# Kernel optimization log

Measured on AMD Instinct MI355X. Metric: run time of the kernel, lower is better.

Reference implementation:

```python
import jax, jax.numpy as jnp
import numpy as np

B, T, C = 4, 2048, 1024
N_HEAD = 16
HEAD_DIM = C // N_HEAD


def setup_inputs() -> dict:
    key = jax.random.key(0)
    k1, k2, k3 = jax.random.split(key, 3)
    x = jax.random.normal(k1, (B, T, C), dtype=jnp.float32)
    w_attn = jax.random.normal(k2, (C, 3 * C), dtype=jnp.float32) * 0.02
    b_attn = jnp.zeros((3 * C,), dtype=jnp.float32)
    # c_proj init stddev = 0.02 / sqrt(2 * n_layer), n_layer = 24
    w_proj = jax.random.normal(k3, (C, C), dtype=jnp.float32) * (0.02 / np.sqrt(48.0))
    b_proj = jnp.zeros((C,), dtype=jnp.float32)
    return {"x": x, "w_attn": w_attn, "b_attn": b_attn,
            "w_proj": w_proj, "b_proj": b_proj}


def reference(x, w_attn, b_attn, w_proj, b_proj):
    Bx, Tx, Cx = x.shape
    scale = 1.0 / jnp.sqrt(jnp.asarray(HEAD_DIM, dtype=x.dtype))
    qkv = x @ w_attn + b_attn                      # [B,T,3C]
    qkv = qkv.reshape(Bx, Tx, 3, N_HEAD, HEAD_DIM)
    q, k, v = qkv[:, :, 0], qkv[:, :, 1], qkv[:, :, 2]  # each [B,T,H,D]
    att = jnp.einsum('bthd,bThd->bhtT', q, k) * scale   # [B,H,T,T]
    mask = jnp.tril(jnp.ones((Tx, Tx), dtype=x.dtype)).reshape(1, 1, Tx, Tx)
    att = att * mask - 1e10 * (1 - mask)
    att = jax.nn.softmax(att, axis=-1)
    y = jnp.einsum('bhtT,bThd->bthd', att, v)      # [B,T,H,D]
    y = y.reshape(Bx, Tx, Cx)
    return y @ w_proj + b_proj
```

## Files before the change

kernel.cpp:

```cpp
#include <hip/hip_runtime.h>
#include <hip/hip_bf16.h>


typedef __attribute__((ext_vector_type(8)))  __bf16 bf16x8;
typedef __attribute__((ext_vector_type(2)))  float  f32x2;
typedef __attribute__((ext_vector_type(4)))  float  f32x4;
typedef __attribute__((ext_vector_type(16))) float  f32x16;
typedef __attribute__((ext_vector_type(4)))  unsigned int u32x4;

#define AS1C(p) ((const __attribute__((address_space(1))) unsigned int*)(p))
#define AS3(p)  ((__attribute__((address_space(3))) unsigned int*)(p))

__device__ __forceinline__ unsigned short f2bfu(float f){
  __hip_bfloat16 h = __float2bfloat16(f);
  return __builtin_bit_cast(unsigned short, h);
}

__device__ __forceinline__ void plswapu(unsigned int &a, unsigned int &b){
  asm("v_permlane32_swap_b32 %0, %1" : "+v"(a), "+v"(b));
}
__device__ __forceinline__ unsigned int cvtpk(float lo, float hi){
  unsigned int r;
  asm("v_cvt_pk_bf16_f32 %0, %1, %2" : "=v"(r) : "v"(lo), "v"(hi));
  return r;
}
__device__ __forceinline__ float max3f(float a, float b, float c){
  float r;
  asm("v_max3_f32 %0, %1, %2, %3" : "=v"(r) : "v"(a), "v"(b), "v"(c));
  return r;
}


__global__ __launch_bounds__(256)
void prep_all(const float* __restrict__ x, __hip_bfloat16* __restrict__ xb,
              const float* __restrict__ w_attn, __hip_bfloat16* __restrict__ wattnT,
              const float* __restrict__ w_proj, __hip_bfloat16* __restrict__ wprojT)
{
  __shared__ float tile[32][33];
  const int idx = blockIdx.x;
  if (idx < 2048){
    const int n4 = 8388608/4;
    for (int i = idx*256 + threadIdx.x; i < n4; i += 2048*256){
      float4 v = reinterpret_cast<const float4*>(x)[i];
      ushort4 u;
      u.x = f2bfu(v.x); u.y = f2bfu(v.y); u.z = f2bfu(v.z); u.w = f2bfu(v.w);
      reinterpret_cast<ushort4*>(xb)[i] = u;
    }
  } else {
    const float* in; __hip_bfloat16* out; int C, R, bx, by;
    if (idx < 5120){
      const int f = idx - 2048;
      in = w_attn; out = wattnT; R = 1024; C = 3072;
      bx = f % 96; by = f / 96;
    } else {
      const int f = idx - 5120;
      in = w_proj; out = wprojT; R = 1024; C = 1024;
      bx = f & 31; by = f >> 5;
    }
    const int tx = threadIdx.x & 31, ty = threadIdx.x >> 5;
    const int c0 = bx*32, r0 = by*32;
    for (int i = ty; i < 32; i += 8)
      tile[i][tx] = in[(size_t)(r0+i)*C + c0 + tx];
    __syncthreads();
    for (int i = ty; i < 32; i += 8)
      out[(size_t)(c0+i)*R + r0 + tx] = __float2bfloat16(tile[tx][i]);
  }
}


#define QSCALE 0.1803368801111244f

__device__ __forceinline__ void stage_ab(const __hip_bfloat16* __restrict__ A,
                                         const __hip_bfloat16* __restrict__ Bt,
                                         int m0, int n0, int K, int kt,
                                         __hip_bfloat16* sA, __hip_bfloat16* sB,
                                         int w, int l)
{
  const int k0 = kt*32;
  #pragma unroll
  for (int qq = 0; qq < 2; ++qq){
    const int c = qq*256 + w*64 + l;
    const int row = c>>2, kc = c&3;
    const int kcs = kc ^ ((row>>1)&3);
    __builtin_amdgcn_global_load_lds(AS1C(A  + (size_t)(m0+row)*K + k0 + 8*kcs),
                                     AS3(sA + (qq*256 + w*64)*8), 16, 0, 0);
    __builtin_amdgcn_global_load_lds(AS1C(Bt + (size_t)(n0+row)*K + k0 + 8*kcs),
                                     AS3(sB + (qq*256 + w*64)*8), 16, 0, 0);
  }
}

template<int EPI>
__global__ __launch_bounds__(256)
void gemm_bf16(const __hip_bfloat16* __restrict__ A,
               const __hip_bfloat16* __restrict__ Bt,
               const float* __restrict__ bias,
               int M, int N, int K,
               __hip_bfloat16* __restrict__ q_s,
               __hip_bfloat16* __restrict__ k_s,
               __hip_bfloat16* __restrict__ vT_s,
               float* __restrict__ outf)
{
  __shared__ __align__(16) __hip_bfloat16 sA[2][128*32];
  __shared__ __align__(16) __hip_bfloat16 sB[2][128*32];
  const int tid = threadIdx.x, w = tid>>6, l = tid&63, g = l>>4, li = l&15;
  const int wm = w>>1, wn = w&1;
  const int sw = (li>>1)&3;

  const int nwg = gridDim.x, cpx = nwg >> 3;
  const int swz = (blockIdx.x & 7)*cpx + (blockIdx.x >> 3);
  const int nbx = N >> 7;
  const int GM = 4, chunk = GM * nbx;
  const int grp = swz / chunk, pos = swz - grp*chunk;
  const int m0 = (grp*GM + (pos & (GM-1)))*128;
  const int n0 = (pos >> 2)*128;

  f32x4 acc[4][4] = {};

  const int NT = K >> 5;
  stage_ab(A, Bt, m0, n0, K, 0, sA[0], sB[0], w, l);
  int cur = 0;

  for (int kt = 0; kt < NT; ++kt){
    __syncthreads();
    if (kt + 1 < NT)
      stage_ab(A, Bt, m0, n0, K, kt+1, sA[cur^1], sB[cur^1], w, l);

    bf16x8 af[4], bfr[4];
    #pragma unroll
    for (int mi = 0; mi < 4; ++mi)
      af[mi] = *reinterpret_cast<const bf16x8*>(sA[cur] + (wm*64 + mi*16 + li)*32 + 8*(g ^ sw));
    #pragma unroll
    for (int ni = 0; ni < 4; ++ni)
      bfr[ni] = *reinterpret_cast<const bf16x8*>(sB[cur] + (wn*64 + ni*16 + li)*32 + 8*(g ^ sw));
    #pragma unroll
    for (int mi = 0; mi < 4; ++mi)
      #pragma unroll
      for (int ni = 0; ni < 4; ++ni)
        acc[mi][ni] = __builtin_amdgcn_mfma_f32_16x16x32_bf16(af[mi], bfr[ni], acc[mi][ni], 0, 0, 0);
    cur ^= 1;
  }

  #pragma unroll
  for (int ni = 0; ni < 4; ++ni){
    const int col = n0 + wn*64 + ni*16 + li;
    const float bv = bias[col];
    #pragma unroll
    for (int mi = 0; mi < 4; ++mi){
      #pragma unroll
      for (int e = 0; e < 4; ++e){
        const int row = m0 + wm*64 + mi*16 + 4*g + e;
        const float val = acc[mi][ni][e] + bv;
        if (EPI == 0){
          const int three = col >> 10, h = (col >> 6) & 15, d = col & 63;
          const int b = row >> 11, t = row & 2047;
          const int bh = b*16 + h;
          if (three == 0)      q_s[((size_t)bh*2048 + t)*64 + d]  = __float2bfloat16(val*QSCALE);
          else if (three == 1) k_s[((size_t)bh*2048 + t)*64 + d]  = __float2bfloat16(val);
          else                 vT_s[((size_t)bh*64 + d)*2048 + t] = __float2bfloat16(val);
        } else {
          outf[(size_t)row*N + col] = val;
        }
      }
    }
  }
}


__device__ __forceinline__ void stage_kv64(const __hip_bfloat16* __restrict__ k_s,
                                           const __hip_bfloat16* __restrict__ vT_s,
                                           size_t base, int j,
                                           __hip_bfloat16* sk, __hip_bfloat16* svt,
                                           int tid)
{
  #pragma unroll
  for (int it = 0; it < 4; ++it){
    const int c = it*128 + tid;
    const int r = c>>3, cc = c&7;
    __builtin_amdgcn_global_load_lds(AS1C(k_s  + base + (size_t)(j*64 + r)*64 + 8*(cc ^ (r&7))),
                                     AS3(sk  + c*8), 16, 0, 0);
    __builtin_amdgcn_global_load_lds(AS1C(vT_s + base + (size_t)r*2048 + j*64 + 8*(cc ^ (r&7))),
                                     AS3(svt + c*8), 16, 0, 0);
  }
}

__device__ __forceinline__ bf16x8 ldtile(const __hip_bfloat16* t, int row, int chunk){
  return *reinterpret_cast<const bf16x8*>(t + row*64 + ((chunk ^ (row&7))*8));
}

__global__ __launch_bounds__(128, 3)
void flash_attn(const __hip_bfloat16* __restrict__ q_s,
                const __hip_bfloat16* __restrict__ k_s,
                const __hip_bfloat16* __restrict__ vT_s,
                __hip_bfloat16* __restrict__ y_s)
{
  __shared__ __align__(16) __hip_bfloat16 sk [2][64*64];
  __shared__ __align__(16) __hip_bfloat16 svt[2][64*64];

  const int tid = threadIdx.x, w = tid>>6, l = tid&63;
  const int lq = l&31, hf = l>>5, h4 = 4*hf;
  const int bid = blockIdx.x;
  const int xcd = bid & 7, sl = (bid>>3) & 7;
  const int v = 31 - (bid >> 6);
  const int bh = xcd*8 + sl;
  const size_t base = (size_t)bh * (2048*64);
  const int b = bh >> 4, hh = bh & 15;

  const int tw = 2*v + w;
  const int jd = v;
  const int qabs = 32*tw + lq;
  const int rel = 32*w + lq;

  bf16x8 qf[4];
  #pragma unroll
  for (int ks = 0; ks < 4; ++ks)
    qf[ks] = *reinterpret_cast<const bf16x8*>(q_s + base + (size_t)qabs*64 + 16*ks + 8*hf);

  f32x16 o0 = {}, o1 = {};
  float mrun = -1e30f, lrun = 0.f;

  stage_kv64(k_s, vT_s, base, 0, sk[0], svt[0], tid);

  #pragma unroll 1
  for (int j = 0; j <= jd; ++j){
    __syncthreads();
    if (j + 1 <= jd)
      stage_kv64(k_s, vT_s, base, j+1, sk[(j+1)&1], svt[(j+1)&1], tid);

    const __hip_bfloat16* skc  = sk[j&1];
    const __hip_bfloat16* svtc = svt[j&1];

    f32x16 s0 = {}, s1 = {};
    __builtin_amdgcn_s_setprio(1);
    #pragma unroll
    for (int ks = 0; ks < 4; ++ks){
      bf16x8 kf0 = ldtile(skc, lq,      2*ks + hf);
      s0 = __builtin_amdgcn_mfma_f32_32x32x16_bf16(kf0, qf[ks], s0, 0, 0, 0);
      bf16x8 kf1 = ldtile(skc, 32 + lq, 2*ks + hf);
      s1 = __builtin_amdgcn_mfma_f32_32x32x16_bf16(kf1, qf[ks], s1, 0, 0, 0);
    }
    __builtin_amdgcn_s_setprio(0);

    f32x2 pf2[16];
    #pragma unroll
    for (int i = 0; i < 8; ++i){
      pf2[i]     = (f32x2){ s0[2*i], s0[2*i+1] };
      pf2[8 + i] = (f32x2){ s1[2*i], s1[2*i+1] };
    }
    if (j == jd){
      #pragma unroll
      for (int i = 0; i < 16; ++i){
        const int a = i >> 3;
        const int r0 = (i & 7)*2, r1 = r0 + 1;
        const int kv0 = 32*a + (r0&3) + 8*(r0>>2) + h4;
        const int kv1 = 32*a + (r1&3) + 8*(r1>>2) + h4;
        pf2[i].x = (kv0 <= rel) ? pf2[i].x : -1e30f;
        pf2[i].y = (kv1 <= rel) ? pf2[i].y : -1e30f;
      }
    }

    #define PFX(K) (((K)&1) ? pf2[(K)>>1].y : pf2[(K)>>1].x)
    float t0 = max3f(PFX(0),PFX(1),PFX(2)),   t1 = max3f(PFX(3),PFX(4),PFX(5));
    float t2 = max3f(PFX(6),PFX(7),PFX(8)),   t3 = max3f(PFX(9),PFX(10),PFX(11));
    float t4 = max3f(PFX(12),PFX(13),PFX(14)),t5 = max3f(PFX(15),PFX(16),PFX(17));
    float t6 = max3f(PFX(18),PFX(19),PFX(20)),t7 = max3f(PFX(21),PFX(22),PFX(23));
    float t8 = max3f(PFX(24),PFX(25),PFX(26)),t9 = max3f(PFX(27),PFX(28),PFX(29));
    float t10 = fmaxf(PFX(30),PFX(31));
    float u0 = max3f(t0,t1,t2), u1 = max3f(t3,t4,t5), u2 = max3f(t6,t7,t8);
    float u3 = fmaxf(t9,t10);
    float pm = fmaxf(max3f(u0,u1,u2), u3);
    #undef PFX

    if (!__all(pm - mrun <= 8.0f)){
      pm = fmaxf(pm, __shfl_xor(pm, 32));
      const float nm = fmaxf(mrun, pm);
      const float corr = exp2f(mrun - nm);
      mrun = nm;
      o0 *= corr; o1 *= corr;
      lrun *= corr;
    }

    const f32x2 negm = { -mrun, -mrun };
    #pragma unroll
    for (int i = 0; i < 16; ++i) pf2[i] = pf2[i] + negm;
    #pragma unroll
    for (int i = 0; i < 16; ++i){
      pf2[i].x = exp2f(pf2[i].x);
      pf2[i].y = exp2f(pf2[i].y);
    }

    f32x2 q8[8];
    #pragma unroll
    for (int i = 0; i < 8; ++i) q8[i] = pf2[i] + pf2[8+i];
    f32x2 q4a = q8[0]+q8[4], q4b = q8[1]+q8[5], q4c = q8[2]+q8[6], q4d = q8[3]+q8[7];
    f32x2 q2a = q4a+q4c, q2b = q4b+q4d;
    f32x2 q1 = q2a+q2b;
    float psum = q1.x + q1.y;
    psum += __shfl_xor(psum, 32);
    lrun += psum;

    unsigned int wds[16];
    #pragma unroll
    for (int k = 0; k < 16; ++k) wds[k] = cvtpk(pf2[k].x, pf2[k].y);
    #pragma unroll
    for (int a = 0; a < 2; ++a)
      #pragma unroll
      for (int bl = 0; bl < 2; ++bl){
        plswapu(wds[a*8 + 4*bl    ], wds[a*8 + 4*bl + 2]);
        plswapu(wds[a*8 + 4*bl + 1], wds[a*8 + 4*bl + 3]);
      }
    bf16x8 pfr[4];
    #pragma unroll
    for (int B = 0; B < 4; ++B){
      u32x4 tt = { wds[4*B], wds[4*B+1], wds[4*B+2], wds[4*B+3] };
      pfr[B] = __builtin_bit_cast(bf16x8, tt);
    }

    __builtin_amdgcn_s_setprio(1);
    #pragma unroll
    for (int ks = 0; ks < 4; ++ks){
      bf16x8 vf0 = ldtile(svtc, lq,      2*ks + hf);
      o0 = __builtin_amdgcn_mfma_f32_32x32x16_bf16(vf0, pfr[ks], o0, 0, 0, 0);
      bf16x8 vf1 = ldtile(svtc, 32 + lq, 2*ks + hf);
      o1 = __builtin_amdgcn_mfma_f32_32x32x16_bf16(vf1, pfr[ks], o1, 0, 0, 0);
    }
    __builtin_amdgcn_s_setprio(0);
  }

  const float inv = 1.f / lrun;
  __hip_bfloat16* yp = y_s + ((size_t)(b*2048 + qabs))*1024 + hh*64;
  #pragma unroll
  for (int i = 0; i < 8; ++i){
    const int d = (2*i & 3) + 8*(i>>1) + h4;
    *reinterpret_cast<unsigned int*>(yp + d)      = cvtpk(o0[2*i]*inv, o0[2*i+1]*inv);
    *reinterpret_cast<unsigned int*>(yp + 32 + d) = cvtpk(o1[2*i]*inv, o1[2*i+1]*inv);
  }
}


extern "C" void kernel_launch(void* const* d_in, const int* in_sizes, int n_in,
                              void* d_out, int out_size, void* d_ws, size_t ws_size,
                              hipStream_t stream)
{
  const float* x      = (const float*)d_in[0];
  const float* w_attn = (const float*)d_in[1];
  const float* b_attn = (const float*)d_in[2];
  const float* w_proj = (const float*)d_in[3];
  const float* b_proj = (const float*)d_in[4];
  float* out = (float*)d_out;
  char* ws = (char*)d_ws;

  __hip_bfloat16* xb     = (__hip_bfloat16*)(ws + 0);
  __hip_bfloat16* wattnT = (__hip_bfloat16*)(ws + 16777216);
  __hip_bfloat16* wprojT = (__hip_bfloat16*)(ws + 23068672);
  __hip_bfloat16* q_s    = (__hip_bfloat16*)(ws + 25165824);
  __hip_bfloat16* k_s    = (__hip_bfloat16*)(ws + 41943040);
  __hip_bfloat16* vT_s   = (__hip_bfloat16*)(ws + 58720256);
  __hip_bfloat16* y_s    = xb;

  prep_all<<<6144, 256, 0, stream>>>(x, xb, w_attn, wattnT, w_proj, wprojT);

  gemm_bf16<0><<<1536, 256, 0, stream>>>(
      xb, wattnT, b_attn, 8192, 3072, 1024, q_s, k_s, vT_s, (float*)nullptr);

  flash_attn<<<2048, 128, 0, stream>>>(q_s, k_s, vT_s, y_s);

  gemm_bf16<1><<<512, 256, 0, stream>>>(
      y_s, wprojT, b_proj, 8192, 1024, 1024,
      (__hip_bfloat16*)nullptr, (__hip_bfloat16*)nullptr, (__hip_bfloat16*)nullptr, out);
}
```

Measured before the change: 198.8 us.

## Software-pipeline flash attention so PV of previous tile overlaps current QK

Restructures the attention loop so each step issues the QK^T MFMAs for the current KV tile together with the PV MFMAs for the previous tile's probabilities. The aim is to hide the softmax latency (exp, reductions, permlane packing) behind matrix work. Probability fragments alternate between two register sets, V^T tiles are triple-buffered in LDS, and a drain step after the loop applies the final PV. This raises register and LDS use, so launch bounds drop from 3 to 2 blocks per CU, trading occupancy for more instruction-level overlap.

```diff
diff --git a/kernel.cpp b/kernel.cpp
--- a/kernel.cpp
+++ b/kernel.cpp
@@ -187,14 +187,14 @@
   return *reinterpret_cast<const bf16x8*>(t + row*64 + ((chunk ^ (row&7))*8));
 }
 
-__global__ __launch_bounds__(128, 3)
+__global__ __launch_bounds__(128, 2)
 void flash_attn(const __hip_bfloat16* __restrict__ q_s,
                 const __hip_bfloat16* __restrict__ k_s,
                 const __hip_bfloat16* __restrict__ vT_s,
                 __hip_bfloat16* __restrict__ y_s)
 {
   __shared__ __align__(16) __hip_bfloat16 sk [2][64*64];
-  __shared__ __align__(16) __hip_bfloat16 svt[2][64*64];
+  __shared__ __align__(16) __hip_bfloat16 svt[3][64*64];
 
   const int tid = threadIdx.x, w = tid>>6, l = tid&63;
   const int lq = l&31, hf = l>>5, h4 = 4*hf;
@@ -217,113 +217,138 @@
 
   f32x16 o0 = {}, o1 = {};
   float mrun = -1e30f, lrun = 0.f;
-
-  stage_kv64(k_s, vT_s, base, 0, sk[0], svt[0], tid);
-
+  bf16x8 pfrA[4], pfrB[4];
+
+  __hip_bfloat16 *skC = sk[0],  *skN = sk[1];
+  __hip_bfloat16 *svP = svt[2], *svC = svt[0], *svN = svt[1];
+
+  stage_kv64(k_s, vT_s, base, 0, skC, svC, tid);
+
+  #define ATTN_STEP(J, PFR_P, PFR_C)                                          \
+  {                                                                           \
+    const int j_ = (J);                                                       \
+    __syncthreads();                                                          \
+    if (j_ + 1 <= jd)                                                         \
+      stage_kv64(k_s, vT_s, base, j_+1, skN, svN, tid);                       \
+    f32x16 s0 = {}, s1 = {};                                                  \
+    __builtin_amdgcn_s_setprio(1);                                            \
+    _Pragma("unroll")                                                         \
+    for (int ks = 0; ks < 4; ++ks){                                           \
+      bf16x8 kf0 = ldtile(skC, lq,      2*ks + hf);                           \
+      s0 = __builtin_amdgcn_mfma_f32_32x32x16_bf16(kf0, qf[ks], s0, 0,0,0);   \
+      bf16x8 kf1 = ldtile(skC, 32 + lq, 2*ks + hf);                           \
+      s1 = __builtin_amdgcn_mfma_f32_32x32x16_bf16(kf1, qf[ks], s1, 0,0,0);   \
+    }                                                                         \
+    if (j_ > 0){                                                              \
+      _Pragma("unroll")                                                       \
+      for (int ks = 0; ks < 4; ++ks){                                         \
+        bf16x8 vf0 = ldtile(svP, lq,      2*ks + hf);                         \
+        o0 = __builtin_amdgcn_mfma_f32_32x32x16_bf16(vf0, PFR_C[ks], o0,0,0,0);\
+        bf16x8 vf1 = ldtile(svP, 32 + lq, 2*ks + hf);                         \
+        o1 = __builtin_amdgcn_mfma_f32_32x32x16_bf16(vf1, PFR_C[ks], o1,0,0,0);\
+      }                                                                       \
+    }                                                                         \
+    __builtin_amdgcn_s_setprio(0);                                            \
+                       \
+    f32x2 pf2[16];                                                            \
+    _Pragma("unroll")                                                         \
+    for (int i = 0; i < 8; ++i){                                              \
+      pf2[i]     = (f32x2){ s0[2*i], s0[2*i+1] };                             \
+      pf2[8 + i] = (f32x2){ s1[2*i], s1[2*i+1] };                             \
+    }                                                                         \
+    if (j_ == jd){                                                            \
+      _Pragma("unroll")                                                       \
+      for (int i = 0; i < 16; ++i){                                           \
+        const int a = i >> 3;                                                 \
+        const int r0i = (i & 7)*2, r1i = r0i + 1;                             \
+        const int kv0 = 32*a + (r0i&3) + 8*(r0i>>2) + h4;                     \
+        const int kv1 = 32*a + (r1i&3) + 8*(r1i>>2) + h4;                     \
+        pf2[i].x = (kv0 <= rel) ? pf2[i].x : -1e30f;                          \
+        pf2[i].y = (kv1 <= rel) ? pf2[i].y : -1e30f;                          \
+      }                                                                       \
+    }                                                                         \
+    float t0 = max3f(PFX(0),PFX(1),PFX(2)),   t1 = max3f(PFX(3),PFX(4),PFX(5));   \
+    float t2 = max3f(PFX(6),PFX(7),PFX(8)),   t3 = max3f(PFX(9),PFX(10),PFX(11)); \
+    float t4 = max3f(PFX(12),PFX(13),PFX(14)),t5 = max3f(PFX(15),PFX(16),PFX(17));\
+    float t6 = max3f(PFX(18),PFX(19),PFX(20)),t7 = max3f(PFX(21),PFX(22),PFX(23));\
+    float t8 = max3f(PFX(24),PFX(25),PFX(26)),t9 = max3f(PFX(27),PFX(28),PFX(29));\
+    float t10 = fmaxf(PFX(30),PFX(31));                                       \
+    float u0 = max3f(t0,t1,t2), u1 = max3f(t3,t4,t5), u2 = max3f(t6,t7,t8);   \
+    float u3 = fmaxf(t9,t10);                                                 \
+    float pm = fmaxf(max3f(u0,u1,u2), u3);                                    \
+    if (!__all(pm - mrun <= 8.0f)){                                           \
+      pm = fmaxf(pm, __shfl_xor(pm, 32));                                     \
+      const float nm = fmaxf(mrun, pm);                                       \
+      const float corr = exp2f(mrun - nm);                                    \
+      mrun = nm;                                                              \
+      o0 *= corr; o1 *= corr;                                                 \
+      lrun *= corr;                                                           \
+    }                                                                         \
+    const f32x2 negm = { -mrun, -mrun };                                      \
+    _Pragma("unroll")                                                         \
+    for (int i = 0; i < 16; ++i) pf2[i] = pf2[i] + negm;                      \
+    _Pragma("unroll")                                                         \
+    for (int i = 0; i < 16; ++i){                                             \
+      pf2[i].x = exp2f(pf2[i].x);                                             \
+      pf2[i].y = exp2f(pf2[i].y);                                             \
+    }                                                                         \
+    f32x2 q8[8];                                                              \
+    _Pragma("unroll")                                                         \
+    for (int i = 0; i < 8; ++i) q8[i] = pf2[i] + pf2[8+i];                    \
+    f32x2 q4a = q8[0]+q8[4], q4b = q8[1]+q8[5], q4c = q8[2]+q8[6], q4d = q8[3]+q8[7];\
+    f32x2 q2a = q4a+q4c, q2b = q4b+q4d;                                       \
+    f32x2 q1 = q2a+q2b;                                                       \
+    float psum = q1.x + q1.y;                                                 \
+    psum += __shfl_xor(psum, 32);                                             \
+    lrun += psum;                                                             \
+    unsigned int wds[16];                                                     \
+    _Pragma("unroll")                                                         \
+    for (int k = 0; k < 16; ++k) wds[k] = cvtpk(pf2[k].x, pf2[k].y);          \
+    _Pragma("unroll")                                                         \
+    for (int a = 0; a < 2; ++a)                                               \
+      _Pragma("unroll")                                                       \
+      for (int bl = 0; bl < 2; ++bl){                                         \
+        plswapu(wds[a*8 + 4*bl    ], wds[a*8 + 4*bl + 2]);                    \
+        plswapu(wds[a*8 + 4*bl + 1], wds[a*8 + 4*bl + 3]);                    \
+      }                                                                       \
+    _Pragma("unroll")                                                         \
+    for (int B = 0; B < 4; ++B){                                              \
+      u32x4 tt = { wds[4*B], wds[4*B+1], wds[4*B+2], wds[4*B+3] };            \
+      PFR_P[B] = __builtin_bit_cast(bf16x8, tt);                              \
+    }                                                                         \
+                 \
+    { __hip_bfloat16* t_ = skC; skC = skN; skN = t_; }                        \
+    { __hip_bfloat16* t_ = svP; svP = svC; svC = svN; svN = t_; }             \
+  }
+
+  #define PFX(K) (((K)&1) ? pf2[(K)>>1].y : pf2[(K)>>1].x)
+  int j = 0;
   #pragma unroll 1
-  for (int j = 0; j <= jd; ++j){
-    __syncthreads();
-    if (j + 1 <= jd)
-      stage_kv64(k_s, vT_s, base, j+1, sk[(j+1)&1], svt[(j+1)&1], tid);
-
-    const __hip_bfloat16* skc  = sk[j&1];
-    const __hip_bfloat16* svtc = svt[j&1];
-
-    f32x16 s0 = {}, s1 = {};
-    __builtin_amdgcn_s_setprio(1);
+  for (; j + 1 <= jd; j += 2){
+    ATTN_STEP(j,   pfrA, pfrB);
+    ATTN_STEP(j+1, pfrB, pfrA);
+  }
+  if (j <= jd)
+    ATTN_STEP(j, pfrA, pfrB);
+  #undef PFX
+  #undef ATTN_STEP
+
+  if ((jd & 1) == 0){
     #pragma unroll
     for (int ks = 0; ks < 4; ++ks){
-      bf16x8 kf0 = ldtile(skc, lq,      2*ks + hf);
-      s0 = __builtin_amdgcn_mfma_f32_32x32x16_bf16(kf0, qf[ks], s0, 0, 0, 0);
-      bf16x8 kf1 = ldtile(skc, 32 + lq, 2*ks + hf);
-      s1 = __builtin_amdgcn_mfma_f32_32x32x16_bf16(kf1, qf[ks], s1, 0, 0, 0);
-    }
-    __builtin_amdgcn_s_setprio(0);
-
-    f32x2 pf2[16];
-    #pragma unroll
-    for (int i = 0; i < 8; ++i){
-      pf2[i]     = (f32x2){ s0[2*i], s0[2*i+1] };
-      pf2[8 + i] = (f32x2){ s1[2*i], s1[2*i+1] };
-    }
-    if (j == jd){
-      #pragma unroll
-      for (int i = 0; i < 16; ++i){
-        const int a = i >> 3;
-        const int r0 = (i & 7)*2, r1 = r0 + 1;
-        const int kv0 = 32*a + (r0&3) + 8*(r0>>2) + h4;
-        const int kv1 = 32*a + (r1&3) + 8*(r1>>2) + h4;
-        pf2[i].x = (kv0 <= rel) ? pf2[i].x : -1e30f;
-        pf2[i].y = (kv1 <= rel) ? pf2[i].y : -1e30f;
-      }
-    }
-
-    #define PFX(K) (((K)&1) ? pf2[(K)>>1].y : pf2[(K)>>1].x)
-    float t0 = max3f(PFX(0),PFX(1),PFX(2)),   t1 = max3f(PFX(3),PFX(4),PFX(5));
-    float t2 = max3f(PFX(6),PFX(7),PFX(8)),   t3 = max3f(PFX(9),PFX(10),PFX(11));
-    float t4 = max3f(PFX(12),PFX(13),PFX(14)),t5 = max3f(PFX(15),PFX(16),PFX(17));
-    float t6 = max3f(PFX(18),PFX(19),PFX(20)),t7 = max3f(PFX(21),PFX(22),PFX(23));
-    float t8 = max3f(PFX(24),PFX(25),PFX(26)),t9 = max3f(PFX(27),PFX(28),PFX(29));
-    float t10 = fmaxf(PFX(30),PFX(31));
-    float u0 = max3f(t0,t1,t2), u1 = max3f(t3,t4,t5), u2 = max3f(t6,t7,t8);
-    float u3 = fmaxf(t9,t10);
-    float pm = fmaxf(max3f(u0,u1,u2), u3);
-    #undef PFX
-
-    if (!__all(pm - mrun <= 8.0f)){
-      pm = fmaxf(pm, __shfl_xor(pm, 32));
-      const float nm = fmaxf(mrun, pm);
-      const float corr = exp2f(mrun - nm);
-      mrun = nm;
-      o0 *= corr; o1 *= corr;
-      lrun *= corr;
-    }
-
-    const f32x2 negm = { -mrun, -mrun };
-    #pragma unroll
-    for (int i = 0; i < 16; ++i) pf2[i] = pf2[i] + negm;
-    #pragma unroll
-    for (int i = 0; i < 16; ++i){
-      pf2[i].x = exp2f(pf2[i].x);
-      pf2[i].y = exp2f(pf2[i].y);
-    }
-
-    f32x2 q8[8];
-    #pragma unroll
-    for (int i = 0; i < 8; ++i) q8[i] = pf2[i] + pf2[8+i];
-    f32x2 q4a = q8[0]+q8[4], q4b = q8[1]+q8[5], q4c = q8[2]+q8[6], q4d = q8[3]+q8[7];
-    f32x2 q2a = q4a+q4c, q2b = q4b+q4d;
-    f32x2 q1 = q2a+q2b;
-    float psum = q1.x + q1.y;
-    psum += __shfl_xor(psum, 32);
-    lrun += psum;
-
-    unsigned int wds[16];
-    #pragma unroll
-    for (int k = 0; k < 16; ++k) wds[k] = cvtpk(pf2[k].x, pf2[k].y);
-    #pragma unroll
-    for (int a = 0; a < 2; ++a)
-      #pragma unroll
-      for (int bl = 0; bl < 2; ++bl){
-        plswapu(wds[a*8 + 4*bl    ], wds[a*8 + 4*bl + 2]);
-        plswapu(wds[a*8 + 4*bl + 1], wds[a*8 + 4*bl + 3]);
-      }
-    bf16x8 pfr[4];
-    #pragma unroll
-    for (int B = 0; B < 4; ++B){
-      u32x4 tt = { wds[4*B], wds[4*B+1], wds[4*B+2], wds[4*B+3] };
-      pfr[B] = __builtin_bit_cast(bf16x8, tt);
-    }
-
-    __builtin_amdgcn_s_setprio(1);
+      bf16x8 vf0 = ldtile(svP, lq,      2*ks + hf);
+      o0 = __builtin_amdgcn_mfma_f32_32x32x16_bf16(vf0, pfrA[ks], o0, 0, 0, 0);
+      bf16x8 vf1 = ldtile(svP, 32 + lq, 2*ks + hf);
+      o1 = __builtin_amdgcn_mfma_f32_32x32x16_bf16(vf1, pfrA[ks], o1, 0, 0, 0);
+    }
+  } else {
     #pragma unroll
     for (int ks = 0; ks < 4; ++ks){
-      bf16x8 vf0 = ldtile(svtc, lq,      2*ks + hf);
-      o0 = __builtin_amdgcn_mfma_f32_32x32x16_bf16(vf0, pfr[ks], o0, 0, 0, 0);
-      bf16x8 vf1 = ldtile(svtc, 32 + lq, 2*ks + hf);
-      o1 = __builtin_amdgcn_mfma_f32_32x32x16_bf16(vf1, pfr[ks], o1, 0, 0, 0);
-    }
-    __builtin_amdgcn_s_setprio(0);
+      bf16x8 vf0 = ldtile(svP, lq,      2*ks + hf);
+      o0 = __builtin_amdgcn_mfma_f32_32x32x16_bf16(vf0, pfrB[ks], o0, 0, 0, 0);
+      bf16x8 vf1 = ldtile(svP, 32 + lq, 2*ks + hf);
+      o1 = __builtin_amdgcn_mfma_f32_32x32x16_bf16(vf1, pfrB[ks], o1, 0, 0, 0);
+    }
   }
 
   const float inv = 1.f / lrun;
```

Result: faster. 186.7 us (median of 2 runs) (-6.1%).
